# Kernel tuning notes

Measured on AMD Instinct MI355X. Metric: run time of the kernel, lower is better.

Reference implementation:

```python
import jax, jax.numpy as jnp
import numpy as np

N_NODES = 50000
N_EDGES = 800000
IN_FEATS = 256
OUT_FEATS = 64


def setup_inputs() -> dict:
    key = jax.random.key(0)
    k1, k2, k3, k4, k5, k6 = jax.random.split(key, 6)
    h = jax.random.normal(k1, (N_NODES, IN_FEATS), dtype=jnp.float32)
    norm = jax.random.uniform(k2, (N_NODES, 1), dtype=jnp.float32)
    weight = jax.random.normal(k3, (IN_FEATS, OUT_FEATS), dtype=jnp.float32) * (1.0 / np.sqrt(OUT_FEATS))
    bias = jax.random.normal(k4, (OUT_FEATS,), dtype=jnp.float32) * (1.0 / np.sqrt(OUT_FEATS))
    src = jax.random.randint(k5, (N_EDGES,), 0, N_NODES, dtype=jnp.int32)
    dst = jax.random.randint(k6, (N_EDGES,), 0, N_NODES, dtype=jnp.int32)
    return {"h": h, "norm": norm, "weight": weight, "bias": bias, "src": src, "dst": dst}


def reference(h, norm, weight, bias, src, dst):
    # h: [N, in_feats] -> linear transform
    hw = h @ weight                      # [N, out_feats]
    hw = hw * norm                       # pre-aggregation norm scale
    # update_all(copy_u, sum): out[v] = sum_{(u,v) in E} hw[u]
    msgs = hw[src]                       # [E, out_feats] gather
    agg = jax.ops.segment_sum(msgs, dst, num_segments=N_NODES)  # [N, out_feats]
    out = agg * norm                     # post-aggregation norm scale
    out = out + bias
    return jax.nn.relu(out)
```

## Files before the change

### kernel.cpp

```cpp
#include <hip/hip_runtime.h>

#define NN 50000
#define NE 800000
#define KF 256
#define MF 64

#define NBK 782
#define HB 49
#define EPB 16384
#define CAP 1536
#define GEMMB 196
#define OVF_CAP 4096

typedef __attribute__((ext_vector_type(8))) short short8;
typedef __attribute__((ext_vector_type(4))) float f32x4;

static __device__ __forceinline__ unsigned short f2bf(float x) {
  unsigned int u = __float_as_uint(x);
  u += 0x7FFF + ((u >> 16) & 1);
  return (unsigned short)(u >> 16);
}
static __device__ __forceinline__ float bf2f(unsigned short u) {
  return __uint_as_float(((unsigned int)u) << 16);
}

__global__ __launch_bounds__(1024) void scatter_gemm(
    const int* __restrict__ src, const int* __restrict__ dst,
    int* __restrict__ gCur, int* __restrict__ gOvf,
    unsigned int* __restrict__ ovf, int* __restrict__ eidx,
    const float* __restrict__ h, const float* __restrict__ W,
    const float* __restrict__ norm, unsigned short* __restrict__ hwb) {
  const int t = threadIdx.x;

  if (blockIdx.x >= HB) {
    __shared__ unsigned short wt[16384];
    for (int f = t; f < 2048; f += 1024) {
      const int m = f & 15;
      const int quad = (f >> 4) & 3;
      const int nt = (f >> 6) & 3;
      const int k0i = f >> 8;
      const int n = nt * 16 + m;
      const int kb = k0i * 32 + quad * 8;
      short8 p;
#pragma unroll
      for (int j = 0; j < 8; ++j) p[j] = (short)f2bf(W[(kb + j) * MF + n]);
      *(short8*)(wt + (size_t)f * 8) = p;
    }

    const int sub = t >> 8;
    const int tt = t & 255;
    const int lane = tt & 63;
    const int wv = tt >> 6;
    const int m = lane & 15;
    const int quad = lane >> 4;
    const int row0 = (blockIdx.x - HB) * 256 + sub * 64;
    const int arow = row0 + wv * 16 + m;
    const int rowc = (arow < NN) ? arow : (NN - 1);
    const float4* ap = (const float4*)(h + (size_t)rowc * KF + quad * 8);

    float4 a[16];
#pragma unroll
    for (int k = 0; k < 8; ++k) {
      a[2 * k] = ap[k * 8];
      a[2 * k + 1] = ap[k * 8 + 1];
    }
    __builtin_amdgcn_sched_barrier(0);

    short8 af[8];
#pragma unroll
    for (int k = 0; k < 8; ++k) {
      const float4 a0 = a[2 * k];
      const float4 a1 = a[2 * k + 1];
      af[k][0] = (short)f2bf(a0.x); af[k][1] = (short)f2bf(a0.y);
      af[k][2] = (short)f2bf(a0.z); af[k][3] = (short)f2bf(a0.w);
      af[k][4] = (short)f2bf(a1.x); af[k][5] = (short)f2bf(a1.y);
      af[k][6] = (short)f2bf(a1.z); af[k][7] = (short)f2bf(a1.w);
    }
    __syncthreads();

    f32x4 acc[4];
#pragma unroll
    for (int i = 0; i < 4; ++i) acc[i] = (f32x4){0.f, 0.f, 0.f, 0.f};

    const short8* wp = (const short8*)wt;
#pragma unroll
    for (int k0i = 0; k0i < 8; ++k0i) {
      const short8* wk = wp + k0i * 256 + lane;
#pragma unroll
      for (int nt = 0; nt < 4; ++nt) {
        const short8 bf = wk[nt * 64];
        acc[nt] = __builtin_amdgcn_mfma_f32_16x16x32_bf16(af[k0i], bf, acc[nt], 0, 0, 0);
      }
    }

    const int gm0 = row0 + wv * 16 + quad * 4;
    float nrm[4];
#pragma unroll
    for (int r = 0; r < 4; ++r) nrm[r] = (gm0 + r < NN) ? norm[gm0 + r] : 0.f;
#pragma unroll
    for (int nt = 0; nt < 4; ++nt) {
#pragma unroll
      for (int r = 0; r < 4; ++r) {
        const int gm = gm0 + r;
        if (gm < NN) hwb[(size_t)gm * MF + nt * 16 + m] = f2bf(acc[nt][r] * nrm[r]);
      }
    }
    return;
  }

  __shared__ int hh[NBK];
  __shared__ int bb[NBK];
  const int base = (int)blockIdx.x * EPB;
  unsigned int ev[EPB / 1024];
#pragma unroll
  for (int i = 0; i < EPB / 1024; ++i) {
    const int e = base + i * 1024 + t;
    ev[i] = (e < NE) ? (((unsigned)src[e] << 16) | (unsigned)dst[e])
                     : 0xFFFFFFFFu;
  }
  for (int i = t; i < NBK; i += 1024) hh[i] = 0;
  __syncthreads();
#pragma unroll
  for (int i = 0; i < EPB / 1024; ++i)
    if (ev[i] != 0xFFFFFFFFu) atomicAdd(&hh[(ev[i] & 0xFFFFu) >> 6], 1);
  __syncthreads();
  for (int i = t; i < NBK; i += 1024) {
    const int c = hh[i];
    bb[i] = c ? atomicAdd(&gCur[i], c) : 0;
  }
  __syncthreads();
#pragma unroll
  for (int i = 0; i < EPB / 1024; ++i) {
    const unsigned v = ev[i];
    if (v != 0xFFFFFFFFu) {
      const int d = (int)(v & 0xFFFFu);
      const int bk = d >> 6;
      const int p = atomicAdd(&bb[bk], 1);
      if (p < CAP) {
        eidx[(size_t)bk * CAP + p] = (int)((v >> 16) << 6) | (d & 63);
      } else {
        const int o = atomicAdd(gOvf, 1);
        if (o < OVF_CAP) ovf[o] = v;
      }
    }
  }
}

__global__ __launch_bounds__(1024) void sort_gather(
    const int* __restrict__ gCur, const int* __restrict__ gOvf,
    const unsigned int* __restrict__ ovf, const int* __restrict__ eidx,
    const unsigned short* __restrict__ hwb, const float* __restrict__ norm,
    const float* __restrict__ bias, float* __restrict__ out) {
  __shared__ int hcnt[64];
  __shared__ int sBeg[64];
  __shared__ int sCur[64];
  __shared__ int sE[CAP];
  const int t = threadIdx.x;
  const int g = blockIdx.x;
  int cnt = gCur[g];
  cnt = (cnt < CAP) ? cnt : CAP;
  cnt = __builtin_amdgcn_readfirstlane(cnt);
  const int* ep = eidx + (size_t)g * CAP;
  if (t < 64) hcnt[t] = 0;
  __syncthreads();
  int v0 = -1, v1 = -1;
  if (t < cnt) {
    v0 = ep[t];
    atomicAdd(&hcnt[v0 & 63], 1);
  }
  if (t + 1024 < cnt) {
    v1 = ep[t + 1024];
    atomicAdd(&hcnt[v1 & 63], 1);
  }
  __syncthreads();
  if (t < 64) {
    const int v = hcnt[t];
    int incl = v;
#pragma unroll
    for (int off = 1; off < 64; off <<= 1) {
      const int u = __shfl_up(incl, off, 64);
      if (t >= off) incl += u;
    }
    sBeg[t] = incl - v;
    sCur[t] = incl - v;
    hcnt[t] = incl;
  }
  __syncthreads();
  if (v0 >= 0) sE[atomicAdd(&sCur[v0 & 63], 1)] = v0 >> 6;
  if (v1 >= 0) sE[atomicAdd(&sCur[v1 & 63], 1)] = v1 >> 6;
  __syncthreads();

  const int lane = t & 63;
  const int wv = t >> 6;
  const float bi = bias[lane];
  const int novf = __builtin_amdgcn_readfirstlane(*gOvf);
#pragma unroll
  for (int nl = wv; nl < 64; nl += 16) {
    const int vtx = (g << 6) + nl;
    if (vtx >= NN) continue;
    const int s0i = __builtin_amdgcn_readfirstlane(sBeg[nl]);
    const int e0i = __builtin_amdgcn_readfirstlane(hcnt[nl]);
    float acc = 0.f;
    int i = s0i;
    for (; i + 8 <= e0i; i += 8) {
      const int s0 = sE[i], s1 = sE[i + 1], s2 = sE[i + 2], s3 = sE[i + 3];
      const int s4 = sE[i + 4], s5 = sE[i + 5], s6 = sE[i + 6], s7 = sE[i + 7];
      const unsigned short x0 = hwb[(size_t)s0 * MF + lane];
      const unsigned short x1 = hwb[(size_t)s1 * MF + lane];
      const unsigned short x2 = hwb[(size_t)s2 * MF + lane];
      const unsigned short x3 = hwb[(size_t)s3 * MF + lane];
      const unsigned short x4 = hwb[(size_t)s4 * MF + lane];
      const unsigned short x5 = hwb[(size_t)s5 * MF + lane];
      const unsigned short x6 = hwb[(size_t)s6 * MF + lane];
      const unsigned short x7 = hwb[(size_t)s7 * MF + lane];
      acc += bf2f(x0); acc += bf2f(x1); acc += bf2f(x2); acc += bf2f(x3);
      acc += bf2f(x4); acc += bf2f(x5); acc += bf2f(x6); acc += bf2f(x7);
    }
    for (; i < e0i; ++i) acc += bf2f(hwb[(size_t)sE[i] * MF + lane]);
    if (novf > 0) {
      const int nn = (novf < OVF_CAP) ? novf : OVF_CAP;
      for (int ii = 0; ii < nn; ++ii) {
        const unsigned v = ovf[ii];
        if ((int)(v & 0xFFFFu) == vtx)
          acc += bf2f(hwb[(size_t)(v >> 16) * MF + lane]);
      }
    }
    const float o = acc * norm[vtx] + bi;
    out[(size_t)vtx * MF + lane] = fmaxf(o, 0.f);
  }
}

extern "C" void kernel_launch(void* const* d_in, const int* in_sizes, int n_in,
                              void* d_out, int out_size, void* d_ws, size_t ws_size,
                              hipStream_t stream) {
  const float* h = (const float*)d_in[0];
  const float* norm = (const float*)d_in[1];
  const float* W = (const float*)d_in[2];
  const float* bias = (const float*)d_in[3];
  const int* src = (const int*)d_in[4];
  const int* dst = (const int*)d_in[5];
  float* out = (float*)d_out;

  unsigned short* hwb = (unsigned short*)d_ws;
  int* gCur = (int*)(hwb + (size_t)NN * MF);
  int* gOvf = gCur + NBK;
  unsigned int* ovf = (unsigned int*)(gOvf + 1);
  int* eidx = (int*)(ovf + OVF_CAP);
  const size_t need = (size_t)NN * MF * 2 +
                      ((size_t)NBK + 1 + OVF_CAP + (size_t)NBK * CAP) * 4;
  if (ws_size < need) return;

  hipMemsetAsync(gCur, 0, (NBK + 1) * sizeof(int), stream);
  scatter_gemm<<<HB + GEMMB, 1024, 0, stream>>>(src, dst, gCur, gOvf, ovf,
                                                eidx, h, W, norm, hwb);
  sort_gather<<<NBK, 1024, 0, stream>>>(gCur, gOvf, ovf, eidx, hwb, norm, bias,
                                        out);
}
```

Baseline: 134.7 us.

## Locally sort edges per block before bucket write and interleave vertex gathers

The scatter phase now uses 196 smaller blocks of 4096 edges each. Every block does a shared-memory prefix sum and a counting sort by destination bucket, then writes each bucket's run to global memory contiguously through wave-cooperative copies, so writes are coalesced instead of random. The gather phase now works on four vertices per wave at once, in 4-edge steps, to keep more independent loads in flight, and adds a launch-bounds occupancy hint. The costs are extra barriers from the serial 10-step block scan, more global atomics on gCur from more blocks, and extra register pressure in the gather.

```diff
diff --git a/kernel.cpp b/kernel.cpp
--- a/kernel.cpp
+++ b/kernel.cpp
@@ -6,8 +6,9 @@
 #define MF 64
 
 #define NBK 782
-#define HB 49
-#define EPB 16384
+#define SB 196
+#define EPB 4096
+#define EPT 4
 #define CAP 1536
 #define GEMMB 196
 #define OVF_CAP 4096
@@ -23,6 +24,16 @@
 static __device__ __forceinline__ float bf2f(unsigned short u) {
   return __uint_as_float(((unsigned int)u) << 16);
 }
+
+union SMem1 {
+  unsigned short wt[16384];
+  struct {
+    int sorted[EPB];
+    int hh[NBK];
+    int bb[NBK];
+    int gbase[NBK];
+  } sc;
+};
 
 __global__ __launch_bounds__(1024) void scatter_gemm(
     const int* __restrict__ src, const int* __restrict__ dst,
@@ -30,10 +41,10 @@
     unsigned int* __restrict__ ovf, int* __restrict__ eidx,
     const float* __restrict__ h, const float* __restrict__ W,
     const float* __restrict__ norm, unsigned short* __restrict__ hwb) {
+  __shared__ SMem1 u;
   const int t = threadIdx.x;
 
-  if (blockIdx.x >= HB) {
-    __shared__ unsigned short wt[16384];
+  if (blockIdx.x >= SB) {
     for (int f = t; f < 2048; f += 1024) {
       const int m = f & 15;
       const int quad = (f >> 4) & 3;
@@ -44,7 +55,7 @@
       short8 p;
 #pragma unroll
       for (int j = 0; j < 8; ++j) p[j] = (short)f2bf(W[(kb + j) * MF + n]);
-      *(short8*)(wt + (size_t)f * 8) = p;
+      *(short8*)(u.wt + (size_t)f * 8) = p;
     }
 
     const int sub = t >> 8;
@@ -53,7 +64,7 @@
     const int wv = tt >> 6;
     const int m = lane & 15;
     const int quad = lane >> 4;
-    const int row0 = (blockIdx.x - HB) * 256 + sub * 64;
+    const int row0 = (blockIdx.x - SB) * 256 + sub * 64;
     const int arow = row0 + wv * 16 + m;
     const int rowc = (arow < NN) ? arow : (NN - 1);
     const float4* ap = (const float4*)(h + (size_t)rowc * KF + quad * 8);
@@ -82,7 +93,7 @@
 #pragma unroll
     for (int i = 0; i < 4; ++i) acc[i] = (f32x4){0.f, 0.f, 0.f, 0.f};
 
-    const short8* wp = (const short8*)wt;
+    const short8* wp = (const short8*)u.wt;
 #pragma unroll
     for (int k0i = 0; k0i < 8; ++k0i) {
       const short8* wk = wp + k0i * 256 + lane;
@@ -108,45 +119,68 @@
     return;
   }
 
-  __shared__ int hh[NBK];
-  __shared__ int bb[NBK];
   const int base = (int)blockIdx.x * EPB;
-  unsigned int ev[EPB / 1024];
-#pragma unroll
-  for (int i = 0; i < EPB / 1024; ++i) {
+  unsigned int ev[EPT];
+#pragma unroll
+  for (int i = 0; i < EPT; ++i) {
     const int e = base + i * 1024 + t;
     ev[i] = (e < NE) ? (((unsigned)src[e] << 16) | (unsigned)dst[e])
                      : 0xFFFFFFFFu;
   }
-  for (int i = t; i < NBK; i += 1024) hh[i] = 0;
-  __syncthreads();
-#pragma unroll
-  for (int i = 0; i < EPB / 1024; ++i)
-    if (ev[i] != 0xFFFFFFFFu) atomicAdd(&hh[(ev[i] & 0xFFFFu) >> 6], 1);
-  __syncthreads();
-  for (int i = t; i < NBK; i += 1024) {
-    const int c = hh[i];
-    bb[i] = c ? atomicAdd(&gCur[i], c) : 0;
-  }
-  __syncthreads();
-#pragma unroll
-  for (int i = 0; i < EPB / 1024; ++i) {
+  for (int i = t; i < NBK; i += 1024) u.sc.hh[i] = 0;
+  __syncthreads();
+#pragma unroll
+  for (int i = 0; i < EPT; ++i)
+    if (ev[i] != 0xFFFFFFFFu) atomicAdd(&u.sc.hh[(ev[i] & 0xFFFFu) >> 6], 1);
+  __syncthreads();
+  for (int off = 1; off < 1024; off <<= 1) {
+    int a = 0;
+    if (t >= off && t < NBK) a = u.sc.hh[t - off];
+    __syncthreads();
+    if (t < NBK) u.sc.hh[t] += a;
+    __syncthreads();
+  }
+  if (t < NBK) {
+    const int incl = u.sc.hh[t];
+    const int excl = t ? u.sc.hh[t - 1] : 0;
+    u.sc.bb[t] = excl;
+    const int c = incl - excl;
+    if (c) u.sc.gbase[t] = atomicAdd(&gCur[t], c);
+  }
+  __syncthreads();
+#pragma unroll
+  for (int i = 0; i < EPT; ++i) {
     const unsigned v = ev[i];
     if (v != 0xFFFFFFFFu) {
       const int d = (int)(v & 0xFFFFu);
-      const int bk = d >> 6;
-      const int p = atomicAdd(&bb[bk], 1);
-      if (p < CAP) {
-        eidx[(size_t)bk * CAP + p] = (int)((v >> 16) << 6) | (d & 63);
+      const int p = atomicAdd(&u.sc.bb[d >> 6], 1);
+      u.sc.sorted[p] = (int)((v >> 16) << 6) | (d & 63);
+    }
+  }
+  __syncthreads();
+  const int wv = t >> 6;
+  const int lane = t & 63;
+  for (int b = wv; b < NBK; b += 16) {
+    const int incl = __builtin_amdgcn_readfirstlane(u.sc.hh[b]);
+    const int excl = __builtin_amdgcn_readfirstlane(b ? u.sc.hh[b - 1] : 0);
+    const int len = incl - excl;
+    if (len == 0) continue;
+    const int gb = __builtin_amdgcn_readfirstlane(u.sc.gbase[b]);
+    for (int off = lane; off < len; off += 64) {
+      const int val = u.sc.sorted[excl + off];
+      const int gp = gb + off;
+      if (gp < CAP) {
+        eidx[(size_t)b * CAP + gp] = val;
       } else {
         const int o = atomicAdd(gOvf, 1);
-        if (o < OVF_CAP) ovf[o] = v;
-      }
-    }
-  }
-}
-
-__global__ __launch_bounds__(1024) void sort_gather(
+        if (o < OVF_CAP)
+          ovf[o] = ((unsigned)(val >> 6) << 16) | (unsigned)(b * 64 + (val & 63));
+      }
+    }
+  }
+}
+
+__global__ __launch_bounds__(1024, 8) void sort_gather(
     const int* __restrict__ gCur, const int* __restrict__ gOvf,
     const unsigned int* __restrict__ ovf, const int* __restrict__ eidx,
     const unsigned short* __restrict__ hwb, const float* __restrict__ norm,
@@ -178,8 +212,8 @@
     int incl = v;
 #pragma unroll
     for (int off = 1; off < 64; off <<= 1) {
-      const int u = __shfl_up(incl, off, 64);
-      if (t >= off) incl += u;
+      const int uu = __shfl_up(incl, off, 64);
+      if (t >= off) incl += uu;
     }
     sBeg[t] = incl - v;
     sCur[t] = incl - v;
@@ -194,29 +228,67 @@
   const int wv = t >> 6;
   const float bi = bias[lane];
   const int novf = __builtin_amdgcn_readfirstlane(*gOvf);
-#pragma unroll
-  for (int nl = wv; nl < 64; nl += 16) {
+
+  int sI[4], eI[4];
+  float ac[4];
+#pragma unroll
+  for (int r = 0; r < 4; ++r) {
+    const int nl = wv + 16 * r;
+    sI[r] = __builtin_amdgcn_readfirstlane(sBeg[nl]);
+    eI[r] = __builtin_amdgcn_readfirstlane(hcnt[nl]);
+    ac[r] = 0.f;
+  }
+  while (true) {
+    int msk = 0;
+    unsigned short x[4][4];
+#pragma unroll
+    for (int r = 0; r < 4; ++r) {
+      if (sI[r] + 4 <= eI[r]) {
+        msk |= 1 << r;
+        const int i0 = sI[r];
+        const int s0 = sE[i0], s1 = sE[i0 + 1], s2 = sE[i0 + 2], s3 = sE[i0 + 3];
+        x[r][0] = hwb[(size_t)s0 * MF + lane];
+        x[r][1] = hwb[(size_t)s1 * MF + lane];
+        x[r][2] = hwb[(size_t)s2 * MF + lane];
+        x[r][3] = hwb[(size_t)s3 * MF + lane];
+      }
+    }
+    if (!msk) break;
+    __builtin_amdgcn_sched_barrier(0);
+#pragma unroll
+    for (int r = 0; r < 4; ++r) {
+      if (msk & (1 << r)) {
+        ac[r] += (bf2f(x[r][0]) + bf2f(x[r][1])) + (bf2f(x[r][2]) + bf2f(x[r][3]));
+        sI[r] += 4;
+      }
+    }
+  }
+  while (true) {
+    int msk = 0;
+    unsigned short y[4];
+#pragma unroll
+    for (int r = 0; r < 4; ++r) {
+      if (sI[r] < eI[r]) {
+        msk |= 1 << r;
+        y[r] = hwb[(size_t)sE[sI[r]] * MF + lane];
+      }
+    }
+    if (!msk) break;
+#pragma unroll
+    for (int r = 0; r < 4; ++r) {
+      if (msk & (1 << r)) {
+        ac[r] += bf2f(y[r]);
+        sI[r] += 1;
+      }
+    }
+  }
+
+#pragma unroll
+  for (int r = 0; r < 4; ++r) {
+    const int nl = wv + 16 * r;
     const int vtx = (g << 6) + nl;
     if (vtx >= NN) continue;
-    const int s0i = __builtin_amdgcn_readfirstlane(sBeg[nl]);
-    const int e0i = __builtin_amdgcn_readfirstlane(hcnt[nl]);
-    float acc = 0.f;
-    int i = s0i;
-    for (; i + 8 <= e0i; i += 8) {
-      const int s0 = sE[i], s1 = sE[i + 1], s2 = sE[i + 2], s3 = sE[i + 3];
-      const int s4 = sE[i + 4], s5 = sE[i + 5], s6 = sE[i + 6], s7 = sE[i + 7];
-      const unsigned short x0 = hwb[(size_t)s0 * MF + lane];
-      const unsigned short x1 = hwb[(size_t)s1 * MF + lane];
-      const unsigned short x2 = hwb[(size_t)s2 * MF + lane];
-      const unsigned short x3 = hwb[(size_t)s3 * MF + lane];
-      const unsigned short x4 = hwb[(size_t)s4 * MF + lane];
-      const unsigned short x5 = hwb[(size_t)s5 * MF + lane];
-      const unsigned short x6 = hwb[(size_t)s6 * MF + lane];
-      const unsigned short x7 = hwb[(size_t)s7 * MF + lane];
-      acc += bf2f(x0); acc += bf2f(x1); acc += bf2f(x2); acc += bf2f(x3);
-      acc += bf2f(x4); acc += bf2f(x5); acc += bf2f(x6); acc += bf2f(x7);
-    }
-    for (; i < e0i; ++i) acc += bf2f(hwb[(size_t)sE[i] * MF + lane]);
+    float acc = ac[r];
     if (novf > 0) {
       const int nn = (novf < OVF_CAP) ? novf : OVF_CAP;
       for (int ii = 0; ii < nn; ++ii) {
@@ -251,7 +323,7 @@
   if (ws_size < need) return;
 
   hipMemsetAsync(gCur, 0, (NBK + 1) * sizeof(int), stream);
-  scatter_gemm<<<HB + GEMMB, 1024, 0, stream>>>(src, dst, gCur, gOvf, ovf,
+  scatter_gemm<<<SB + GEMMB, 1024, 0, stream>>>(src, dst, gCur, gOvf, ovf,
                                                 eidx, h, W, norm, hwb);
   sort_gather<<<NBK, 1024, 0, stream>>>(gCur, gOvf, ovf, eidx, hwb, norm, bias,
                                         out);
```

After: 152.8 us. +13.4%, slower.
